# Kernel optimization log

Hardware: AMD Instinct MI355X
Metric: run time of the kernel (lower is better)

The kernel has to match this reference:

```python
import jax, jax.numpy as jnp
import numpy as np

B, S, R, H = 32, 512, 49, 768


def setup_inputs() -> dict:
    key = jax.random.key(0)
    ks = jax.random.split(key, 32)
    rn = lambda i, shape, s=1.0: jax.random.normal(ks[i], shape, dtype=jnp.float32) * s
    W = 0.05  # weight init scale to keep tanh/softmax in a sane range
    return {
        'text_features': rn(0, (B, S, H)),
        'img_features': rn(1, (B, R, H)),
        't1_w': rn(2, (H, H), W), 't1_b': rn(3, (H,), W),
        'i1_w': rn(4, (H, H), W),
        'a1_w': rn(5, (2 * H,), W), 'a1_b': rn(6, (), W),
        't2_w': rn(7, (H, H), W),
        'i2_w': rn(8, (H, H), W), 'i2_b': rn(9, (H,), W),
        'a2_w': rn(10, (2 * H,), W), 'a2_b': rn(11, (), W),
        'gt_w': rn(12, (H, H), W), 'gt_b': rn(13, (H,), W),
        'gi_w': rn(14, (H, H), W), 'gi_b': rn(15, (H,), W),
        'gg_w': rn(16, (2 * H, 1), W), 'gg_b': rn(17, (1,), W),
        'ft_w': rn(18, (H, H), W),
        'fm_w': rn(19, (H, H), W), 'fm_b': rn(20, (H,), W),
        'fg_w': rn(21, (2 * H, 1), W), 'fg_b': rn(22, (1,), W),
        'fr_w': rn(23, (H, H), W), 'fr_b': rn(24, (H,), W),
    }


def reference(text_features, img_features, t1_w, t1_b, i1_w, a1_w, a1_b,
              t2_w, i2_w, i2_b, a2_w, a2_b, gt_w, gt_b, gi_w, gi_b,
              gg_w, gg_b, ft_w, fm_w, fm_b, fg_w, fg_b, fr_w, fr_b):
    H = text_features.shape[-1]
    # --- CoAttention, stage 1 (text attends over image regions) ---
    # tanh(concat) is elementwise and att_linear_1 is rank-1, so split the score:
    # score[b,s,r] = tanh(t1(x_s)) . a1[:H] + tanh(i1(y_r)) . a1[H:] + b
    t_sc = jnp.tanh(text_features @ t1_w + t1_b) @ a1_w[:H]          # (B,S)
    i_sc = jnp.tanh(img_features @ i1_w) @ a1_w[H:]                  # (B,R)
    visual_att = jax.nn.softmax(t_sc[:, :, None] + i_sc[:, None, :] + a1_b, axis=-1)  # (B,S,R)
    att_img = jnp.einsum('bsr,brh->bsh', visual_att, img_features)   # (B,S,H)
    # --- CoAttention, stage 2 (attended-image queries attend over text) ---
    # concat order is [img, text] -> a2[:H] pairs with img part
    q_sc = jnp.tanh(att_img @ i2_w + i2_b) @ a2_w[:H]                # (B,S)
    k_sc = jnp.tanh(text_features @ t2_w) @ a2_w[H:]                 # (B,S)
    textual_att = jax.nn.softmax(q_sc[:, :, None] + k_sc[:, None, :] + a2_b, axis=-1)  # (B,S,S)
    att_text = jnp.einsum('bij,bjh->bih', textual_att, text_features)  # (B,S,H)
    # --- GMF gated fusion ---
    new_img = jnp.tanh(att_img @ gi_w + gi_b)
    new_txt = jnp.tanh(att_text @ gt_w + gt_b)
    gate = jax.nn.sigmoid(jnp.concatenate([new_img, new_txt], axis=-1) @ gg_w + gg_b)  # (B,S,1)
    multimodal = gate * new_img + (1.0 - gate) * new_txt
    # --- filtration gate ---
    concat_feat = jnp.concatenate([text_features @ ft_w, multimodal @ fm_w + fm_b], axis=-1)
    fgate = jax.nn.sigmoid(concat_feat @ fg_w + fg_b)                # (B,S,1)
    return fgate * jnp.tanh(multimodal @ fr_w + fr_b)
```

## Files before the change

kernel.cpp:

```cpp
#include <hip/hip_runtime.h>
#include <hip/hip_bf16.h>
#include <math.h>

constexpr int BD = 32;
constexpr int SD = 512;
constexpr int RD = 49;
constexpr int HD = 768;
constexpr int MT = BD * SD;
constexpr int MI = BD * RD;
constexpr int NP = 6;
constexpr int MBT3 = MT / 256;
constexpr int MBI3 = 7;
constexpr int NB3 = 3;
constexpr int NWG3 = (MBT3 + MBI3) * NB3;
constexpr int NT3 = HD / 64;

typedef __bf16 bf16;
typedef __bf16 bf16x4 __attribute__((ext_vector_type(4)));
typedef __bf16 bf16x8 __attribute__((ext_vector_type(8)));
typedef float f32x4 __attribute__((ext_vector_type(4)));

#define GLOAD_LDS16(g, l) __builtin_amdgcn_global_load_lds( \
    (__attribute__((address_space(1))) void*)(g),           \
    (__attribute__((address_space(3))) void*)(l), 16, 0, 0)
#define BAR() __builtin_amdgcn_s_barrier()
#define SCHED_FENCE() __builtin_amdgcn_sched_barrier(0)
#define WAITV(n) asm volatile("s_waitcnt vmcnt(" #n ")" ::: "memory")

__device__ __forceinline__ float fast_tanh(float x) {
    const float e = __expf(2.f * x);
    return 1.f - 2.f / (e + 1.f);
}

__global__ __launch_bounds__(256) void prep_text(
    const float* __restrict__ text, const float* __restrict__ v_f,
    bf16* __restrict__ text_bf, float* __restrict__ s_txt)
{
    const int row = blockIdx.x * 4 + (threadIdx.x >> 6);
    const int lane = threadIdx.x & 63;
    const float* tr = text + (size_t)row * HD;
    bf16* tb = text_bf + (size_t)row * HD;
    float acc = 0.f;
    #pragma unroll
    for (int c = 0; c < 3; ++c) {
        const int o = c * 256 + lane * 4;
        const f32x4 x = *(const f32x4*)(tr + o);
        const f32x4 v = *(const f32x4*)(v_f + o);
        bf16x4 b; b[0] = (bf16)x[0]; b[1] = (bf16)x[1]; b[2] = (bf16)x[2]; b[3] = (bf16)x[3];
        *(bf16x4*)(tb + o) = b;
        acc += x[0] * v[0] + x[1] * v[1] + x[2] * v[2] + x[3] * v[3];
    }
    for (int off = 32; off; off >>= 1) acc += __shfl_xor(acc, off);
    if (lane == 0) s_txt[row] = acc;
}

__global__ __launch_bounds__(256) void prep_misc(
    const float* __restrict__ ft_w, const float* __restrict__ fm_w,
    const float* __restrict__ fm_b, const float* __restrict__ fg_w,
    float* __restrict__ v_f, float* __restrict__ v_m, float* __restrict__ c_m,
    const float* __restrict__ img, bf16* __restrict__ img_bf,
    const float* __restrict__ t2_w, const float* __restrict__ i1_w,
    bf16* __restrict__ wt_t, bf16* __restrict__ wt_i)
{
    __shared__ float tile[64][65];
    const int bid = blockIdx.x;
    if (bid < 385) {
        const int idx = bid * 4 + (threadIdx.x >> 6);
        const int lane = threadIdx.x & 63;
        const float* row; const float* vecp; float* outp;
        if (idx < HD)            { row = ft_w + (size_t)idx * HD;        vecp = fg_w;      outp = v_f + idx; }
        else if (idx < 2 * HD)   { row = fm_w + (size_t)(idx - HD) * HD; vecp = fg_w + HD; outp = v_m + (idx - HD); }
        else if (idx == 2 * HD)  { row = fm_b;                           vecp = fg_w + HD; outp = c_m; }
        else return;
        float acc = 0.f;
        #pragma unroll
        for (int i = 0; i < HD / 64; ++i) acc += row[lane + 64 * i] * vecp[lane + 64 * i];
        for (int off = 32; off; off >>= 1) acc += __shfl_xor(acc, off);
        if (lane == 0) *outp = acc;
    } else if (bid < 385 + 588) {
        const int i = (bid - 385) * 256 + threadIdx.x;
        const int n8 = BD * RD * HD / 8;
        if (i >= n8) return;
        const size_t o = (size_t)i * 8;
        const f32x4 x0 = *(const f32x4*)(img + o);
        const f32x4 x1 = *(const f32x4*)(img + o + 4);
        bf16x8 b;
        b[0]=(bf16)x0[0]; b[1]=(bf16)x0[1]; b[2]=(bf16)x0[2]; b[3]=(bf16)x0[3];
        b[4]=(bf16)x1[0]; b[5]=(bf16)x1[1]; b[6]=(bf16)x1[2]; b[7]=(bf16)x1[3];
        *(bf16x8*)(img_bf + o) = b;
    } else {
        const int idx2 = bid - (385 + 588);
        const int z = idx2 / 144, rem = idx2 % 144;
        const int bx = rem % 12, by = rem / 12;
        const float* W = z ? i1_w : t2_w;
        bf16* Wt = z ? wt_i : wt_t;
        const int k0 = bx * 64, n0 = by * 64;
        const int t = threadIdx.x;
        const int rb = t >> 6, c = t & 63;
        #pragma unroll
        for (int i = 0; i < 16; ++i) {
            const int r = rb + i * 4;
            tile[r][c] = W[(size_t)(k0 + r) * HD + n0 + c];
        }
        __syncthreads();
        #pragma unroll
        for (int i = 0; i < 16; ++i) {
            const int r = rb + i * 4;
            Wt[(size_t)(n0 + r) * HD + k0 + c] = (bf16)tile[c][r];
        }
    }
}

__global__ __launch_bounds__(512, 2) void gemm3(
    const bf16* __restrict__ Atext, const bf16* __restrict__ WtT,
    const float* __restrict__ vecT, float* __restrict__ partT,
    const bf16* __restrict__ Aimg, const bf16* __restrict__ WtI,
    const float* __restrict__ vecI, float* __restrict__ partI)
{
    __shared__ __align__(16) bf16 As[2 * 16384];
    __shared__ __align__(16) bf16 Bs[2 * 16384];

    const int bid = blockIdx.x;
    const int q = NWG3 / 8, r = NWG3 % 8;
    const int xcd = bid % 8, sidx = bid / 8;
    const int o = (xcd < r ? xcd * (q + 1) : r * (q + 1) + (xcd - r) * q) + sidx;
    const int mb = o / NB3, nb = o % NB3;

    const bool isT = mb < MBT3;
    const bf16* A    = isT ? Atext : Aimg;
    const bf16* Wt   = isT ? WtT : WtI;
    const float* vec = isT ? vecT : vecI;
    float* part      = isT ? partT : partI;
    const int m0 = (isT ? mb : mb - MBT3) * 256;
    const int n0 = nb * 256;

    const int t = threadIdx.x;
    const int w = t >> 6, lane = t & 63;
    const int quad = lane >> 4, l16 = lane & 15;
    const int wm_idx = w & 3, wn_idx = w >> 2;
    const int wm2 = wm_idx * 64, wn2 = wn_idx * 128;

    const bf16* Ag = A  + (size_t)(m0 + l16) * HD + quad * 8;
    const bf16* Bg = Wt + (size_t)(n0 + l16) * HD + quad * 8;

    f32x4 acc[4][8] = {};

#define STAGE3(tt, bb) {                                                     \
    const int kk = (tt) * 64;                                                \
    _Pragma("unroll")                                                        \
    for (int h = 0; h < 2; ++h) {                                            \
        _Pragma("unroll")                                                    \
        for (int j = 0; j < 2; ++j) {                                        \
            const int rc = 2 * w + j;                                        \
            GLOAD_LDS16(Ag + (size_t)rc * 16 * HD + kk + h * 32,             \
                        As + (bb) * 16384 + (h * 16 + rc) * 512);            \
            GLOAD_LDS16(Bg + (size_t)rc * 16 * HD + kk + h * 32,             \
                        Bs + (bb) * 16384 + (h * 16 + rc) * 512);            \
        }                                                                    \
    }                                                                        \
}

#define COMPUTE3(bb) {                                                       \
    _Pragma("unroll")                                                        \
    for (int h = 0; h < 2; ++h) {                                            \
        bf16x8 af[4], bg[8];                                                 \
        _Pragma("unroll")                                                    \
        for (int fi = 0; fi < 4; ++fi)                                       \
            af[fi] = *(const bf16x8*)(As + (bb) * 16384 +                    \
                       (h * 16 + wm_idx * 4 + fi) * 512 + lane * 8);         \
        _Pragma("unroll")                                                    \
        for (int fj = 0; fj < 8; ++fj)                                       \
            bg[fj] = *(const bf16x8*)(Bs + (bb) * 16384 +                    \
                       (h * 16 + wn_idx * 8 + fj) * 512 + lane * 8);         \
        _Pragma("unroll")                                                    \
        for (int fi = 0; fi < 4; ++fi)                                       \
            _Pragma("unroll")                                                \
            for (int fj = 0; fj < 8; ++fj)                                   \
                acc[fi][fj] = __builtin_amdgcn_mfma_f32_16x16x32_bf16(       \
                    af[fi], bg[fj], acc[fi][fj], 0, 0, 0);                   \
    }                                                                        \
}

    STAGE3(0, 0);
    for (int tt = 0; tt < NT3 - 1; ++tt) {
        STAGE3(tt + 1, (tt + 1) & 1);
        WAITV(8);
        BAR();
        SCHED_FENCE();
        COMPUTE3(tt & 1);
        SCHED_FENCE();
        BAR();
    }
    WAITV(0);
    BAR();
    SCHED_FENCE();
    COMPUTE3((NT3 - 1) & 1);

#undef STAGE3
#undef COMPUTE3

    float vv[8];
    #pragma unroll
    for (int fj = 0; fj < 8; ++fj) vv[fj] = vec[n0 + wn2 + fj * 16 + l16];

    #pragma unroll
    for (int fi = 0; fi < 4; ++fi) {
        #pragma unroll
        for (int reg = 0; reg < 4; ++reg) {
            float p = 0.f;
            #pragma unroll
            for (int fj = 0; fj < 8; ++fj)
                p += fast_tanh(acc[fi][fj][reg]) * vv[fj];
            p += __shfl_xor(p, 1);
            p += __shfl_xor(p, 2);
            p += __shfl_xor(p, 4);
            p += __shfl_xor(p, 8);
            if (l16 == 0) {
                const int row = m0 + wm2 + fi * 16 + quad * 4 + reg;
                part[(size_t)row * NP + nb * 2 + wn_idx] = p;
            }
        }
    }
}

__global__ __launch_bounds__(256) void wsum2(
    const float* __restrict__ k_part, const float* __restrict__ i_part,
    const bf16* __restrict__ text_bf, const float* __restrict__ img,
    float* __restrict__ atxt, float* __restrict__ aimg)
{
    __shared__ float S[SD];
    __shared__ float red[4];
    const int bid = blockIdx.x;
    const bool isText = bid < 96;
    const int idx = isText ? bid : bid - 96;
    const int b = idx & 31, hy = idx >> 5;
    const int t = threadIdx.x;

    if (isText) {
        for (int j = t; j < SD; j += 256) {
            const float* p = k_part + (size_t)(b * SD + j) * NP;
            float s = 0.f;
            #pragma unroll
            for (int u = 0; u < NP; ++u) s += p[u];
            S[j] = s;
        }
        __syncthreads();
        float m = fmaxf(S[t], S[t + 256]);
        for (int off = 32; off; off >>= 1) m = fmaxf(m, __shfl_xor(m, off));
        if ((t & 63) == 0) red[t >> 6] = m;
        __syncthreads();
        m = fmaxf(fmaxf(red[0], red[1]), fmaxf(red[2], red[3]));
        float lsum = 0.f;
        {
            const float e0 = __expf(S[t] - m), e1 = __expf(S[t + 256] - m);
            S[t] = e0; S[t + 256] = e1;
            lsum = e0 + e1;
        }
        for (int off = 32; off; off >>= 1) lsum += __shfl_xor(lsum, off);
        __syncthreads();
        if ((t & 63) == 0) red[t >> 6] = lsum;
        __syncthreads();
        const float inv = 1.f / (red[0] + red[1] + red[2] + red[3]);
        const int h = hy * 256 + t;
        const bf16* Xb = text_bf + (size_t)b * SD * HD + h;
        float acc = 0.f;
        #pragma unroll 8
        for (int j = 0; j < SD; ++j) acc += S[j] * (float)Xb[(size_t)j * HD];
        atxt[b * HD + h] = acc * inv;
    } else {
        if (t < 64) {
            float s0 = -1e30f;
            if (t < RD) {
                const float* p = i_part + (size_t)(b * RD + t) * NP;
                float s = 0.f;
                #pragma unroll
                for (int u = 0; u < NP; ++u) s += p[u];
                s0 = s;
            }
            float m = s0;
            for (int off = 32; off; off >>= 1) m = fmaxf(m, __shfl_xor(m, off));
            float e = (t < RD) ? __expf(s0 - m) : 0.f;
            float lsum = e;
            for (int off = 32; off; off >>= 1) lsum += __shfl_xor(lsum, off);
            if (t < RD) S[t] = e;
            if (t == 0) red[0] = 1.f / lsum;
        }
        __syncthreads();
        const float inv = red[0];
        const int h = hy * 256 + t;
        const float* Xb = img + (size_t)b * RD * HD + h;
        float acc = 0.f;
        #pragma unroll 7
        for (int j = 0; j < RD; ++j) acc += S[j] * Xb[(size_t)j * HD];
        aimg[b * HD + h] = acc * inv;
    }
}

__global__ __launch_bounds__(256) void ni_nt_kernel(
    const float* __restrict__ aimg, const float* __restrict__ atxt,
    const float* __restrict__ gi_w, const float* __restrict__ gi_b,
    const float* __restrict__ gt_w, const float* __restrict__ gt_b,
    float* __restrict__ ni, float* __restrict__ nt)
{
    const int b = blockIdx.x, n0 = blockIdx.y * 64, which = blockIdx.z;
    const float* X = which ? atxt : aimg;
    const float* W = which ? gt_w : gi_w;
    const float* bias = which ? gt_b : gi_b;
    float* Y = which ? nt : ni;

    __shared__ float Xs[HD];
    __shared__ float partial[4][64];
    const int t = threadIdx.x;
    for (int h = t; h < HD; h += 256) Xs[h] = X[b * HD + h];
    __syncthreads();
    const int n = n0 + (t & 63), kq = t >> 6;
    float acc = 0.f;
    const float* Wp = W + (size_t)(kq * 192) * HD + n;
    #pragma unroll 8
    for (int h = 0; h < 192; ++h) acc += Xs[kq * 192 + h] * Wp[(size_t)h * HD];
    partial[kq][t & 63] = acc;
    __syncthreads();
    if (t < 64) {
        const float s = partial[0][t] + partial[1][t] + partial[2][t] + partial[3][t];
        Y[b * HD + n0 + t] = tanhf(s + bias[n0 + t]);
    }
}

__global__ __launch_bounds__(256) void gateT(
    const float* __restrict__ ni, const float* __restrict__ nt,
    const float* __restrict__ gg_w, const float* __restrict__ gg_b,
    const float* __restrict__ v_m, const float* __restrict__ c_m,
    const float* __restrict__ fg_b,
    const float* __restrict__ fr_w, const float* __restrict__ fr_b,
    float* __restrict__ T, float* __restrict__ s_mm)
{
    const int b = blockIdx.x, n0 = blockIdx.y * 64, t = threadIdx.x;
    __shared__ float Ni[HD], Nt[HD], Mm[HD];
    __shared__ float partial[4][64];
    __shared__ float red[4];
    __shared__ float gsh;

    float acc = 0.f;
    for (int n = t; n < HD; n += 256) {
        const float vi = ni[b * HD + n], vt = nt[b * HD + n];
        Ni[n] = vi; Nt[n] = vt;
        acc += vi * gg_w[n] + vt * gg_w[HD + n];
    }
    for (int off = 32; off; off >>= 1) acc += __shfl_xor(acc, off);
    if ((t & 63) == 0) red[t >> 6] = acc;
    __syncthreads();
    if (t == 0) gsh = 1.f / (1.f + expf(-(red[0] + red[1] + red[2] + red[3] + gg_b[0])));
    __syncthreads();
    const float g = gsh;
    float a2 = 0.f;
    for (int n = t; n < HD; n += 256) {
        const float m = g * Ni[n] + (1.f - g) * Nt[n];
        Mm[n] = m;
        a2 += m * v_m[n];
    }
    __syncthreads();
    const int n = n0 + (t & 63), kq = t >> 6;
    float tacc = 0.f;
    const float* Wp = fr_w + (size_t)(kq * 192) * HD + n;
    #pragma unroll 8
    for (int h = 0; h < 192; ++h) tacc += Mm[kq * 192 + h] * Wp[(size_t)h * HD];
    partial[kq][t & 63] = tacc;
    if (blockIdx.y == 0) {
        for (int off = 32; off; off >>= 1) a2 += __shfl_xor(a2, off);
        __syncthreads();
        if ((t & 63) == 0) red[t >> 6] = a2;
        __syncthreads();
        if (t == 0) s_mm[b] = red[0] + red[1] + red[2] + red[3] + *c_m + fg_b[0];
    } else {
        __syncthreads();
    }
    __syncthreads();
    if (t < 64) {
        const float s = partial[0][t] + partial[1][t] + partial[2][t] + partial[3][t];
        T[b * HD + n0 + t] = tanhf(s + fr_b[n0 + t]);
    }
}

__global__ __launch_bounds__(256) void out_kernel(const float* __restrict__ s_txt,
                                                  const float* __restrict__ s_mm,
                                                  const float* __restrict__ T,
                                                  float* __restrict__ out) {
    const size_t idx = ((size_t)blockIdx.x * 256 + threadIdx.x) * 4;
    const int h = (int)(idx % HD);
    const int bs = (int)(idx / HD);
    const int b = bs >> 9;
    float f = s_txt[bs] + s_mm[b];
    f = 1.f / (1.f + expf(-f));
    const float* Tp = T + b * HD + h;
    f32x4 o;
    o[0] = f * Tp[0]; o[1] = f * Tp[1]; o[2] = f * Tp[2]; o[3] = f * Tp[3];
    *(f32x4*)(out + idx) = o;
}

extern "C" void kernel_launch(void* const* d_in, const int* in_sizes, int n_in,
                              void* d_out, int out_size, void* d_ws, size_t ws_size,
                              hipStream_t stream) {
    const float* text = (const float*)d_in[0];
    const float* img  = (const float*)d_in[1];
    const float* i1_w = (const float*)d_in[4];
    const float* a1_w = (const float*)d_in[5];
    const float* t2_w = (const float*)d_in[7];
    const float* a2_w = (const float*)d_in[10];
    const float* gt_w = (const float*)d_in[12];
    const float* gt_b = (const float*)d_in[13];
    const float* gi_w = (const float*)d_in[14];
    const float* gi_b = (const float*)d_in[15];
    const float* gg_w = (const float*)d_in[16];
    const float* gg_b = (const float*)d_in[17];
    const float* ft_w = (const float*)d_in[18];
    const float* fm_w = (const float*)d_in[19];
    const float* fm_b = (const float*)d_in[20];
    const float* fg_w = (const float*)d_in[21];
    const float* fg_b = (const float*)d_in[22];
    const float* fr_w = (const float*)d_in[23];
    const float* fr_b = (const float*)d_in[24];
    float* out = (float*)d_out;

    float* sc_ = out;
    float* i_part  = sc_;
    float* k_part  = sc_ + 38400;
    float* aimg    = sc_ + 449600;
    float* atxt    = sc_ + 474176;
    float* v_f     = sc_ + 498752;
    float* v_m     = sc_ + 499520;
    float* c_m     = sc_ + 500288;
    float* ni      = sc_ + 598656;
    float* nt      = sc_ + 623232;
    bf16* text_bf  = (bf16*)(sc_ + 672384);
    bf16* img_bf   = (bf16*)(sc_ + 6963840);
    bf16* wt_t     = (bf16*)(sc_ + 7565952);
    bf16* wt_i     = (bf16*)(sc_ + 7860864);

    float* ws    = (float*)d_ws;
    float* s_txt = ws;
    float* s_mm  = ws + 16384;
    float* T     = ws + 16448;

    prep_misc<<<dim3(385 + 588 + 288), dim3(256), 0, stream>>>(
        ft_w, fm_w, fm_b, fg_w, v_f, v_m, c_m, img, img_bf, t2_w, i1_w, wt_t, wt_i);
    prep_text<<<dim3(MT / 4), dim3(256), 0, stream>>>(text, v_f, text_bf, s_txt);
    gemm3<<<dim3(NWG3), dim3(512), 0, stream>>>(
        text_bf, wt_t, a2_w + HD, k_part, img_bf, wt_i, a1_w + HD, i_part);
    wsum2<<<dim3(192), dim3(256), 0, stream>>>(
        k_part, i_part, text_bf, img, atxt, aimg);
    ni_nt_kernel<<<dim3(BD, HD / 64, 2), dim3(256), 0, stream>>>(
        aimg, atxt, gi_w, gi_b, gt_w, gt_b, ni, nt);
    gateT<<<dim3(BD, HD / 64), dim3(256), 0, stream>>>(
        ni, nt, gg_w, gg_b, v_m, c_m, fg_b, fr_w, fr_b, T, s_mm);
    out_kernel<<<dim3((MT * HD / 4) / 256), dim3(256), 0, stream>>>(s_txt, s_mm, T, out);
}
```

Measured before the change: 271.8 us.

## Split text weighted-sum over sequence quarters and vectorize small GEMV kernels

```diff
diff --git a/kernel.cpp b/kernel.cpp
--- a/kernel.cpp
+++ b/kernel.cpp
@@ -223,26 +223,22 @@
     }
 }
 
-__global__ __launch_bounds__(256) void wsum2(
+__global__ __launch_bounds__(256) void wsum3(
     const float* __restrict__ k_part, const float* __restrict__ i_part,
     const bf16* __restrict__ text_bf, const float* __restrict__ img,
-    float* __restrict__ atxt, float* __restrict__ aimg)
+    float* __restrict__ at_part, float* __restrict__ aimg)
 {
     __shared__ float S[SD];
     __shared__ float red[4];
+    __shared__ float P2[2][96][8];
     const int bid = blockIdx.x;
-    const bool isText = bid < 96;
-    const int idx = isText ? bid : bid - 96;
-    const int b = idx & 31, hy = idx >> 5;
     const int t = threadIdx.x;
 
-    if (isText) {
+    if (bid < 128) {
+        const int b = bid >> 2, jq = bid & 3;
         for (int j = t; j < SD; j += 256) {
             const float* p = k_part + (size_t)(b * SD + j) * NP;
-            float s = 0.f;
-            #pragma unroll
-            for (int u = 0; u < NP; ++u) s += p[u];
-            S[j] = s;
+            S[j] = p[0] + p[1] + p[2] + p[3] + p[4] + p[5];
         }
         __syncthreads();
         float m = fmaxf(S[t], S[t + 256]);
@@ -250,32 +246,48 @@
         if ((t & 63) == 0) red[t >> 6] = m;
         __syncthreads();
         m = fmaxf(fmaxf(red[0], red[1]), fmaxf(red[2], red[3]));
-        float lsum = 0.f;
-        {
-            const float e0 = __expf(S[t] - m), e1 = __expf(S[t + 256] - m);
-            S[t] = e0; S[t + 256] = e1;
-            lsum = e0 + e1;
-        }
+        const float e0 = __expf(S[t] - m), e1 = __expf(S[t + 256] - m);
+        S[t] = e0; S[t + 256] = e1;
+        float lsum = e0 + e1;
         for (int off = 32; off; off >>= 1) lsum += __shfl_xor(lsum, off);
         __syncthreads();
         if ((t & 63) == 0) red[t >> 6] = lsum;
         __syncthreads();
         const float inv = 1.f / (red[0] + red[1] + red[2] + red[3]);
-        const int h = hy * 256 + t;
-        const bf16* Xb = text_bf + (size_t)b * SD * HD + h;
-        float acc = 0.f;
-        #pragma unroll 8
-        for (int j = 0; j < SD; ++j) acc += S[j] * (float)Xb[(size_t)j * HD];
-        atxt[b * HD + h] = acc * inv;
+        const int o = t % 96, jh = t / 96;
+        if (jh < 2) {
+            float a[8] = {};
+            const bf16* Xb = text_bf + ((size_t)b * SD + jq * 128 + jh * 64) * HD + o * 8;
+            const float* Sp = S + jq * 128 + jh * 64;
+            #pragma unroll 8
+            for (int jj = 0; jj < 64; ++jj) {
+                const bf16x8 v = *(const bf16x8*)(Xb + (size_t)jj * HD);
+                const float s = Sp[jj];
+                #pragma unroll
+                for (int e = 0; e < 8; ++e) a[e] += s * (float)v[e];
+            }
+            #pragma unroll
+            for (int e = 0; e < 8; ++e) P2[jh][o][e] = a[e];
+        }
+        __syncthreads();
+        if (t < 96) {
+            float* dst = at_part + ((size_t)(b * 4 + jq)) * HD + t * 8;
+            f32x4 o0, o1;
+            #pragma unroll
+            for (int e = 0; e < 4; ++e) o0[e] = (P2[0][t][e] + P2[1][t][e]) * inv;
+            #pragma unroll
+            for (int e = 0; e < 4; ++e) o1[e] = (P2[0][t][e + 4] + P2[1][t][e + 4]) * inv;
+            *(f32x4*)dst = o0;
+            *(f32x4*)(dst + 4) = o1;
+        }
     } else {
+        const int idx = bid - 128;
+        const int b = idx & 31, hy = idx >> 5;
         if (t < 64) {
             float s0 = -1e30f;
             if (t < RD) {
                 const float* p = i_part + (size_t)(b * RD + t) * NP;
-                float s = 0.f;
-                #pragma unroll
-                for (int u = 0; u < NP; ++u) s += p[u];
-                s0 = s;
+                s0 = p[0] + p[1] + p[2] + p[3] + p[4] + p[5];
             }
             float m = s0;
             for (int off = 32; off; off >>= 1) m = fmaxf(m, __shfl_xor(m, off));
@@ -296,37 +308,50 @@
     }
 }
 
-__global__ __launch_bounds__(256) void ni_nt_kernel(
-    const float* __restrict__ aimg, const float* __restrict__ atxt,
+__global__ __launch_bounds__(256) void ni_nt3(
+    const float* __restrict__ aimg, const float* __restrict__ at_part,
     const float* __restrict__ gi_w, const float* __restrict__ gi_b,
     const float* __restrict__ gt_w, const float* __restrict__ gt_b,
     float* __restrict__ ni, float* __restrict__ nt)
 {
-    const int b = blockIdx.x, n0 = blockIdx.y * 64, which = blockIdx.z;
-    const float* X = which ? atxt : aimg;
+    const int b = blockIdx.x, n0 = blockIdx.y * 128, which = blockIdx.z;
     const float* W = which ? gt_w : gi_w;
     const float* bias = which ? gt_b : gi_b;
     float* Y = which ? nt : ni;
 
     __shared__ float Xs[HD];
-    __shared__ float partial[4][64];
+    __shared__ float part[8][32][4];
     const int t = threadIdx.x;
-    for (int h = t; h < HD; h += 256) Xs[h] = X[b * HD + h];
-    __syncthreads();
-    const int n = n0 + (t & 63), kq = t >> 6;
-    float acc = 0.f;
-    const float* Wp = W + (size_t)(kq * 192) * HD + n;
-    #pragma unroll 8
-    for (int h = 0; h < 192; ++h) acc += Xs[kq * 192 + h] * Wp[(size_t)h * HD];
-    partial[kq][t & 63] = acc;
-    __syncthreads();
-    if (t < 64) {
-        const float s = partial[0][t] + partial[1][t] + partial[2][t] + partial[3][t];
-        Y[b * HD + n0 + t] = tanhf(s + bias[n0 + t]);
-    }
-}
-
-__global__ __launch_bounds__(256) void gateT(
+    if (which) {
+        for (int h = t; h < HD; h += 256)
+            Xs[h] = at_part[((size_t)(b * 4 + 0)) * HD + h] + at_part[((size_t)(b * 4 + 1)) * HD + h]
+                  + at_part[((size_t)(b * 4 + 2)) * HD + h] + at_part[((size_t)(b * 4 + 3)) * HD + h];
+    } else {
+        for (int h = t; h < HD; h += 256) Xs[h] = aimg[b * HD + h];
+    }
+    __syncthreads();
+    const int lane32 = t & 31, kq = t >> 5;
+    const int n = n0 + lane32 * 4;
+    f32x4 acc = {0.f, 0.f, 0.f, 0.f};
+    const float* Wp = W + (size_t)(kq * 96) * HD + n;
+    #pragma unroll 4
+    for (int k = 0; k < 96; ++k) {
+        const f32x4 wv = *(const f32x4*)(Wp + (size_t)k * HD);
+        const float x = Xs[kq * 96 + k];
+        acc[0] += x * wv[0]; acc[1] += x * wv[1];
+        acc[2] += x * wv[2]; acc[3] += x * wv[3];
+    }
+    *(f32x4*)&part[kq][lane32][0] = acc;
+    __syncthreads();
+    if (t < 128) {
+        float s = 0.f;
+        #pragma unroll
+        for (int q2 = 0; q2 < 8; ++q2) s += part[q2][t >> 2][t & 3];
+        Y[b * HD + n0 + t] = fast_tanh(s + bias[n0 + t]);
+    }
+}
+
+__global__ __launch_bounds__(256) void gateT3(
     const float* __restrict__ ni, const float* __restrict__ nt,
     const float* __restrict__ gg_w, const float* __restrict__ gg_b,
     const float* __restrict__ v_m, const float* __restrict__ c_m,
@@ -334,50 +359,52 @@
     const float* __restrict__ fr_w, const float* __restrict__ fr_b,
     float* __restrict__ T, float* __restrict__ s_mm)
 {
-    const int b = blockIdx.x, n0 = blockIdx.y * 64, t = threadIdx.x;
-    __shared__ float Ni[HD], Nt[HD], Mm[HD];
-    __shared__ float partial[4][64];
+    const int b = blockIdx.x, n0 = blockIdx.y * 128, t = threadIdx.x;
+    __shared__ float Mm[HD];
+    __shared__ float part[8][32][4];
     __shared__ float red[4];
     __shared__ float gsh;
 
-    float acc = 0.f;
-    for (int n = t; n < HD; n += 256) {
-        const float vi = ni[b * HD + n], vt = nt[b * HD + n];
-        Ni[n] = vi; Nt[n] = vt;
-        acc += vi * gg_w[n] + vt * gg_w[HD + n];
-    }
-    for (int off = 32; off; off >>= 1) acc += __shfl_xor(acc, off);
-    if ((t & 63) == 0) red[t >> 6] = acc;
+    float accg = 0.f;
+    for (int n = t; n < HD; n += 256)
+        accg += ni[b * HD + n] * gg_w[n] + nt[b * HD + n] * gg_w[HD + n];
+    for (int off = 32; off; off >>= 1) accg += __shfl_xor(accg, off);
+    if ((t & 63) == 0) red[t >> 6] = accg;
     __syncthreads();
     if (t == 0) gsh = 1.f / (1.f + expf(-(red[0] + red[1] + red[2] + red[3] + gg_b[0])));
     __syncthreads();
     const float g = gsh;
     float a2 = 0.f;
     for (int n = t; n < HD; n += 256) {
-        const float m = g * Ni[n] + (1.f - g) * Nt[n];
+        const float m = g * ni[b * HD + n] + (1.f - g) * nt[b * HD + n];
         Mm[n] = m;
         a2 += m * v_m[n];
     }
     __syncthreads();
-    const int n = n0 + (t & 63), kq = t >> 6;
-    float tacc = 0.f;
-    const float* Wp = fr_w + (size_t)(kq * 192) * HD + n;
-    #pragma unroll 8
-    for (int h = 0; h < 192; ++h) tacc += Mm[kq * 192 + h] * Wp[(size_t)h * HD];
-    partial[kq][t & 63] = tacc;
+    const int lane32 = t & 31, kq = t >> 5;
+    const int n = n0 + lane32 * 4;
+    f32x4 acc = {0.f, 0.f, 0.f, 0.f};
+    const float* Wp = fr_w + (size_t)(kq * 96) * HD + n;
+    #pragma unroll 4
+    for (int k = 0; k < 96; ++k) {
+        const f32x4 wv = *(const f32x4*)(Wp + (size_t)k * HD);
+        const float x = Mm[kq * 96 + k];
+        acc[0] += x * wv[0]; acc[1] += x * wv[1];
+        acc[2] += x * wv[2]; acc[3] += x * wv[3];
+    }
+    *(f32x4*)&part[kq][lane32][0] = acc;
     if (blockIdx.y == 0) {
         for (int off = 32; off; off >>= 1) a2 += __shfl_xor(a2, off);
-        __syncthreads();
         if ((t & 63) == 0) red[t >> 6] = a2;
-        __syncthreads();
-        if (t == 0) s_mm[b] = red[0] + red[1] + red[2] + red[3] + *c_m + fg_b[0];
-    } else {
-        __syncthreads();
-    }
-    __syncthreads();
-    if (t < 64) {
-        const float s = partial[0][t] + partial[1][t] + partial[2][t] + partial[3][t];
-        T[b * HD + n0 + t] = tanhf(s + fr_b[n0 + t]);
+    }
+    __syncthreads();
+    if (blockIdx.y == 0 && t == 0)
+        s_mm[b] = red[0] + red[1] + red[2] + red[3] + *c_m + fg_b[0];
+    if (t < 128) {
+        float s = 0.f;
+        #pragma unroll
+        for (int q2 = 0; q2 < 8; ++q2) s += part[q2][t >> 2][t & 3];
+        T[b * HD + n0 + t] = fast_tanh(s + fr_b[n0 + t]);
     }
 }
 
@@ -425,10 +452,10 @@
     float* i_part  = sc_;
     float* k_part  = sc_ + 38400;
     float* aimg    = sc_ + 449600;
-    float* atxt    = sc_ + 474176;
     float* v_f     = sc_ + 498752;
     float* v_m     = sc_ + 499520;
     float* c_m     = sc_ + 500288;
+    float* at_part = sc_ + 500352;
     float* ni      = sc_ + 598656;
     float* nt      = sc_ + 623232;
     bf16* text_bf  = (bf16*)(sc_ + 672384);
@@ -446,11 +473,11 @@
     prep_text<<<dim3(MT / 4), dim3(256), 0, stream>>>(text, v_f, text_bf, s_txt);
     gemm3<<<dim3(NWG3), dim3(512), 0, stream>>>(
         text_bf, wt_t, a2_w + HD, k_part, img_bf, wt_i, a1_w + HD, i_part);
-    wsum2<<<dim3(192), dim3(256), 0, stream>>>(
-        k_part, i_part, text_bf, img, atxt, aimg);
-    ni_nt_kernel<<<dim3(BD, HD / 64, 2), dim3(256), 0, stream>>>(
-        aimg, atxt, gi_w, gi_b, gt_w, gt_b, ni, nt);
-    gateT<<<dim3(BD, HD / 64), dim3(256), 0, stream>>>(
+    wsum3<<<dim3(224), dim3(256), 0, stream>>>(
+        k_part, i_part, text_bf, img, at_part, aimg);
+    ni_nt3<<<dim3(BD, 6, 2), dim3(256), 0, stream>>>(
+        aimg, at_part, gi_w, gi_b, gt_w, gt_b, ni, nt);
+    gateT3<<<dim3(BD, 6), dim3(256), 0, stream>>>(
         ni, nt, gg_w, gg_b, v_m, c_m, fg_b, fr_w, fr_b, T, s_mm);
     out_kernel<<<dim3((MT * HD / 4) / 256), dim3(256), 0, stream>>>(s_txt, s_mm, T, out);
 }
```

Result: faster. 252.6 us (-7.1%).
